# Kernel optimization log

Measured on AMD Instinct MI355X. Metric: run time of the kernel, lower is better.

## Reference

```python
import jax, jax.numpy as jnp
import numpy as np

V = 20000
E = 40000
NODE_IN = 74
EDGE_IN = 12
D = 64            # node_out_feats
EH = 128          # edge_hidden_feats
STEPS = 6         # num_step_message_passing


def setup_inputs() -> dict:
    key = jax.random.key(0)
    ks = jax.random.split(key, 16)
    s = lambda k, shape, scale=0.05: jax.random.normal(k, shape, dtype=jnp.float32) * scale
    return {
        "node_feats": jax.random.normal(ks[0], (V, NODE_IN), dtype=jnp.float32),
        "edge_feats": jax.random.normal(ks[1], (E, EDGE_IN), dtype=jnp.float32),
        "src": jax.random.randint(ks[2], (E,), 0, V),
        "dst": jax.random.randint(ks[3], (E,), 0, V),
        # project_node_feats: Linear(NODE_IN, D) + ReLU
        "proj_W": s(ks[4], (D, NODE_IN)),
        "proj_b": jnp.zeros((D,), jnp.float32),
        # NNConv edge network: Linear(EDGE_IN, EH) -> ReLU -> Linear(EH, D*D)
        "en_W1": s(ks[5], (EH, EDGE_IN)),
        "en_b1": jnp.zeros((EH,), jnp.float32),
        "en_W2": s(ks[6], (D * D, EH)),
        "en_b2": jnp.zeros((D * D,), jnp.float32),
        # NNConv output bias
        "conv_b": jnp.zeros((D,), jnp.float32),
        # single-layer GRU (PyTorch gate order r, z, n)
        "gru_Wih": s(ks[7], (3 * D, D)),
        "gru_Whh": s(ks[8], (3 * D, D)),
        "gru_bih": jnp.zeros((3 * D,), jnp.float32),
        "gru_bhh": jnp.zeros((3 * D,), jnp.float32),
        # MLPPredictor: Linear(2*D, 1)
        "pred_W": s(ks[9], (1, 2 * D)),
        "pred_b": jnp.zeros((1,), jnp.float32),
    }


def reference(node_feats, edge_feats, src, dst, proj_W, proj_b,
              en_W1, en_b1, en_W2, en_b2, conv_b,
              gru_Wih, gru_Whh, gru_bih, gru_bhh, pred_W, pred_b):
    nV = node_feats.shape[0]
    # project node features
    h = jax.nn.relu(node_feats @ proj_W.T + proj_b)  # (V, D)
    # per-edge weight matrices from the edge network (constant across steps)
    ew = jax.nn.relu(edge_feats @ en_W1.T + en_b1) @ en_W2.T + en_b2  # (E, D*D)
    ew = ew.reshape(-1, D, D)  # (E, D, D)

    def step(h, _):
        # NNConv (aggregator='sum'): m_e = h[src_e] @ W_e, sum at dst, + bias
        m = jnp.einsum('ei,eio->eo', h[src], ew)               # (E, D)
        neigh = jax.ops.segment_sum(m, dst, num_segments=nV)   # (V, D)
        x = jax.nn.relu(neigh + conv_b)
        # GRU update; hidden == h (they coincide in the original loop)
        gi = x @ gru_Wih.T + gru_bih
        gh = h @ gru_Whh.T + gru_bhh
        i_r, i_z, i_n = jnp.split(gi, 3, axis=-1)
        h_r, h_z, h_n = jnp.split(gh, 3, axis=-1)
        r = jax.nn.sigmoid(i_r + h_r)
        z = jax.nn.sigmoid(i_z + h_z)
        n = jnp.tanh(i_n + r * h_n)
        h_new = (1.0 - z) * n + z * h
        return h_new, None

    h, _ = jax.lax.scan(step, h, None, length=STEPS)
    # MLPPredictor: per-edge gather-concat-linear
    score = jnp.concatenate([h[src], h[dst]], axis=1) @ pred_W.T + pred_b  # (E, 1)
    return score
```

## Files before the change

### kernel.cpp

```cpp
#include <hip/hip_runtime.h>
#include <hip/hip_bf16.h>
#include <cstdint>

#define NV 20000
#define NE 40000
#define NODE_IN 74
#define EDGE_IN 12
#define D 64
#define EHID 128
#define NSTEPS 6

typedef __bf16 bf16x8 __attribute__((ext_vector_type(8)));
typedef float f32x4 __attribute__((ext_vector_type(4)));

__global__ __launch_bounds__(256) void k_prep(
    const float* __restrict__ nf, const float* __restrict__ pjW, const float* __restrict__ pjb,
    float* __restrict__ h, float* __restrict__ neigh,
    const float* __restrict__ ef, const float* __restrict__ W1, const float* __restrict__ b1,
    __hip_bfloat16* __restrict__ t_bf,
    const float* __restrict__ W2, __hip_bfloat16* __restrict__ w2b,
    const float* __restrict__ b2, __hip_bfloat16* __restrict__ b2t,
    const float* __restrict__ Wih, const float* __restrict__ Whh,
    __hip_bfloat16* __restrict__ Bhi, __hip_bfloat16* __restrict__ Blo) {
  __shared__ float smem[4 * NODE_IN];
  int tid = threadIdx.x;
  int bx = blockIdx.x;
  if (bx < 5000) {
    int nb = bx * 4;
    for (int idx = tid; idx < 4 * NODE_IN; idx += 256)
      smem[idx] = nf[(size_t)nb * NODE_IN + idx];
    __syncthreads();
    int nl = tid >> 6, o = tid & 63;
    float acc = pjb[o];
#pragma unroll
    for (int i = 0; i < NODE_IN; ++i) acc = fmaf(smem[nl * NODE_IN + i], pjW[o * NODE_IN + i], acc);
    h[(size_t)(nb + nl) * D + o] = fmaxf(acc, 0.f);
    neigh[(size_t)(nb + nl) * D + o] = 0.f;
  } else if (bx < 25000) {
    int eb = (bx - 5000) * 2;
    if (tid < 2 * EDGE_IN)
      smem[tid] = ef[(size_t)eb * EDGE_IN + tid];
    __syncthreads();
    int el = tid >> 7, k = tid & 127;
    float acc = b1[k];
#pragma unroll
    for (int j = 0; j < EDGE_IN; ++j) acc = fmaf(smem[el * EDGE_IN + j], W1[k * EDGE_IN + j], acc);
    t_bf[(size_t)(eb + el) * EHID + k] = __float2bfloat16(fmaxf(acc, 0.f));
  } else if (bx < 27048) {
    int idx = (bx - 25000) * 256 + tid;
    w2b[idx] = __float2bfloat16(W2[idx]);
  } else if (bx < 27064) {
    int idx = (bx - 27048) * 256 + tid;
    int o = idx >> 6, i = idx & 63;
    b2t[o * 64 + i] = __float2bfloat16(b2[i * 64 + o]);
  } else {
    int idx = (bx - 27064) * 256 + tid;
    int n = idx >> 7, k = idx & 127;
    int o = n & 63, cls = n >> 6;
    float v;
    if (cls == 0)      v = (k < 64) ? Wih[o * 64 + k]         : Whh[o * 64 + (k - 64)];
    else if (cls == 1) v = (k < 64) ? Wih[(64 + o) * 64 + k]  : Whh[(64 + o) * 64 + (k - 64)];
    else if (cls == 2) v = (k < 64) ? Wih[(128 + o) * 64 + k] : 0.f;
    else               v = (k < 64) ? 0.f                     : Whh[(128 + o) * 64 + (k - 64)];
    __hip_bfloat16 hi = __float2bfloat16(v);
    Bhi[idx] = hi;
    Blo[idx] = __float2bfloat16(v - __bfloat162float(hi));
  }
}

__global__ __launch_bounds__(768, 3) void k_msg(const float* __restrict__ h,
                                                const __hip_bfloat16* __restrict__ t_bf,
                                                const __hip_bfloat16* __restrict__ w2,
                                                const __hip_bfloat16* __restrict__ b2t,
                                                const int* __restrict__ src,
                                                const int* __restrict__ dst,
                                                float* __restrict__ neigh) {
  __shared__ __hip_bfloat16 W2s[512 * 128];
  __shared__ __hip_bfloat16 Hs[12][16 * 64];
  int tid = threadIdx.x;
  int bx = blockIdx.x;
  int cg = bx >> 6, ih = (bx >> 5) & 1, s = bx & 31;
  int lane = tid & 63, lr = lane & 15, lq = lane >> 4;
  int wave = tid >> 6;
  const int ocol = cg * 16 + lr;

  for (int chunk = tid; chunk < 8192; chunk += 768) {
    int row = chunk >> 4, c = chunk & 15;
    int ig = row >> 4, ol = row & 15;
    const __hip_bfloat16* gp =
        w2 + ((size_t)((ih * 32 + ig) * 64 + cg * 16 + ol)) * EHID + c * 8;
    *(bf16x8*)(W2s + row * 128 + ((c ^ ol) * 8)) = *(const bf16x8*)gp;
  }
  bf16x8 b2f0, b2f1;
#pragma unroll
  for (int j = 0; j < 8; ++j) {
    int k = lq * 8 + j;
    __bf16 v = *(const __bf16*)(b2t + (size_t)ocol * 64 + ih * 32 + k);
    __bf16 z = (__bf16)0.0f;
    b2f0[j] = (k < 16) ? v : z;
    b2f1[j] = (k >= 16) ? v : z;
  }
  __syncthreads();

  __hip_bfloat16* Hsw = &Hs[wave][0];
  int e0s = s * 1280;
  int nt = (s < 31) ? 20 : 5;

  int sw0 = (((0 * 4 + lq) ^ lr) * 8);
  int sw1 = (((1 * 4 + lq) ^ lr) * 8);
  int sw2 = (((2 * 4 + lq) ^ lr) * 8);
  int sw3 = (((3 * 4 + lq) ^ lr) * 8);

  int se0 = (wave < nt) ? src[e0s + wave * 64 + lane] : 0;
  int se1 = (wave + 12 < nt) ? src[e0s + (wave + 12) * 64 + lane] : 0;

#pragma unroll 1
  for (int r2 = 0; r2 < 2; ++r2) {
    int t = r2 * 12 + wave;
    if (t >= nt) break;
    int e0t = e0s + t * 64;
    int s_e = r2 ? se1 : se0;

    bf16x8 tf[4][4];
#pragma unroll
    for (int mt = 0; mt < 4; ++mt)
#pragma unroll
      for (int ks = 0; ks < 4; ++ks)
        tf[mt][ks] = *(const bf16x8*)(t_bf + (size_t)(e0t + mt * 16 + lr) * EHID +
                                      ks * 32 + lq * 8);

    int4 dv[4];
#pragma unroll
    for (int mt = 0; mt < 4; ++mt)
      dv[mt] = *(const int4*)(dst + e0t + mt * 16 + lq * 4);

    const float* hrow = h + (size_t)s_e * D + ih * 32;
    f32x4 C[4];
#pragma unroll
    for (int mt = 0; mt < 4; ++mt) C[mt] = f32x4{0.f, 0.f, 0.f, 0.f};

#pragma unroll
    for (int ph = 0; ph < 2; ++ph) {
#pragma unroll
      for (int q = 0; q < 4; ++q) {
        float4 hv = *(const float4*)(hrow + ph * 16 + q * 4);
        Hsw[(q * 4 + 0) * 64 + lane] = __float2bfloat16(hv.x);
        Hsw[(q * 4 + 1) * 64 + lane] = __float2bfloat16(hv.y);
        Hsw[(q * 4 + 2) * 64 + lane] = __float2bfloat16(hv.z);
        Hsw[(q * 4 + 3) * 64 + lane] = __float2bfloat16(hv.w);
      }
#pragma unroll
      for (int mt = 0; mt < 4; ++mt) {
        bf16x8 af;
#pragma unroll
        for (int j = 0; j < 8; ++j)
          af[j] = *(const __bf16*)(Hsw + ((lq * 8 + j) & 15) * 64 + mt * 16 + lr);
        C[mt] = __builtin_amdgcn_mfma_f32_16x16x32_bf16(af, ph ? b2f1 : b2f0, C[mt], 0, 0, 0);
      }
      __builtin_amdgcn_s_setprio(1);
#pragma unroll 2
      for (int igl = 0; igl < 16; ++igl) {
        int ig = ph * 16 + igl;
        const __hip_bfloat16* Wr = W2s + (ig * 16 + lr) * 128;
        bf16x8 f0 = *(const bf16x8*)(Wr + sw0);
        bf16x8 f1 = *(const bf16x8*)(Wr + sw1);
        bf16x8 f2 = *(const bf16x8*)(Wr + sw2);
        bf16x8 f3 = *(const bf16x8*)(Wr + sw3);
#pragma unroll
        for (int mt = 0; mt < 4; ++mt) {
          f32x4 P = {0.f, 0.f, 0.f, 0.f};
          P = __builtin_amdgcn_mfma_f32_16x16x32_bf16(tf[mt][0], f0, P, 0, 0, 0);
          P = __builtin_amdgcn_mfma_f32_16x16x32_bf16(tf[mt][1], f1, P, 0, 0, 0);
          P = __builtin_amdgcn_mfma_f32_16x16x32_bf16(tf[mt][2], f2, P, 0, 0, 0);
          P = __builtin_amdgcn_mfma_f32_16x16x32_bf16(tf[mt][3], f3, P, 0, 0, 0);
          uint2 hA = *(const uint2*)(Hsw + igl * 64 + mt * 16 + lq * 4);
          C[mt][0] = fmaf(__uint_as_float(hA.x << 16), P[0], C[mt][0]);
          C[mt][1] = fmaf(__uint_as_float(hA.x & 0xffff0000u), P[1], C[mt][1]);
          C[mt][2] = fmaf(__uint_as_float(hA.y << 16), P[2], C[mt][2]);
          C[mt][3] = fmaf(__uint_as_float(hA.y & 0xffff0000u), P[3], C[mt][3]);
        }
      }
      __builtin_amdgcn_s_setprio(0);
    }
#pragma unroll
    for (int mt = 0; mt < 4; ++mt) {
      atomicAdd(neigh + (size_t)dv[mt].x * D + ocol, C[mt][0]);
      atomicAdd(neigh + (size_t)dv[mt].y * D + ocol, C[mt][1]);
      atomicAdd(neigh + (size_t)dv[mt].z * D + ocol, C[mt][2]);
      atomicAdd(neigh + (size_t)dv[mt].w * D + ocol, C[mt][3]);
    }
  }
}

__global__ __launch_bounds__(256) void k_gru(float* __restrict__ neigh,
                                             float* __restrict__ h,
                                             const __hip_bfloat16* __restrict__ Bhi,
                                             const __hip_bfloat16* __restrict__ Blo,
                                             const float* __restrict__ cb,
                                             const float* __restrict__ bih,
                                             const float* __restrict__ bhh) {
  __shared__ __hip_bfloat16 Ahi[32 * 128];
  __shared__ __hip_bfloat16 Alo[32 * 128];
  int tid = threadIdx.x;
  int n0 = blockIdx.x * 32;
  for (int idx = tid; idx < 32 * 64; idx += 256) {
    int node = idx >> 6, f = idx & 63;
    int gn = n0 + node;
    float xv = fmaxf(neigh[(size_t)gn * D + f] + cb[f], 0.f);
    neigh[(size_t)gn * D + f] = 0.f;
    float hv = h[(size_t)gn * D + f];
    __hip_bfloat16 xh = __float2bfloat16(xv);
    __hip_bfloat16 hh = __float2bfloat16(hv);
    Ahi[node * 128 + f] = xh;
    Ahi[node * 128 + 64 + f] = hh;
    Alo[node * 128 + f] = __float2bfloat16(xv - __bfloat162float(xh));
    Alo[node * 128 + 64 + f] = __float2bfloat16(hv - __bfloat162float(hh));
  }
  __syncthreads();
  int wave = tid >> 6, lane = tid & 63;
  int lr = lane & 15, lq = lane >> 4;
  f32x4 acc[2][4] = {};
#pragma unroll
  for (int ks = 0; ks < 4; ++ks) {
    int koff = ks * 32 + lq * 8;
    bf16x8 ah[2], al[2], bh[4], bl[4];
#pragma unroll
    for (int mt = 0; mt < 2; ++mt) {
      ah[mt] = *(const bf16x8*)(Ahi + (mt * 16 + lr) * 128 + koff);
      al[mt] = *(const bf16x8*)(Alo + (mt * 16 + lr) * 128 + koff);
    }
#pragma unroll
    for (int cls = 0; cls < 4; ++cls) {
      int n = cls * 64 + wave * 16 + lr;
      bh[cls] = *(const bf16x8*)(Bhi + (size_t)n * 128 + koff);
      bl[cls] = *(const bf16x8*)(Blo + (size_t)n * 128 + koff);
    }
#pragma unroll
    for (int mt = 0; mt < 2; ++mt)
#pragma unroll
      for (int cls = 0; cls < 4; ++cls) {
        acc[mt][cls] = __builtin_amdgcn_mfma_f32_16x16x32_bf16(ah[mt], bh[cls], acc[mt][cls], 0, 0, 0);
        acc[mt][cls] = __builtin_amdgcn_mfma_f32_16x16x32_bf16(al[mt], bh[cls], acc[mt][cls], 0, 0, 0);
        acc[mt][cls] = __builtin_amdgcn_mfma_f32_16x16x32_bf16(ah[mt], bl[cls], acc[mt][cls], 0, 0, 0);
      }
  }
  int o = wave * 16 + lr;
  float b_r = bih[o] + bhh[o];
  float b_z = bih[64 + o] + bhh[64 + o];
  float b_in = bih[128 + o];
  float b_hn = bhh[128 + o];
#pragma unroll
  for (int mt = 0; mt < 2; ++mt) {
#pragma unroll
    for (int r = 0; r < 4; ++r) {
      int gn = n0 + mt * 16 + lq * 4 + r;
      float rs = acc[mt][0][r] + b_r;
      float zs = acc[mt][1][r] + b_z;
      float inn = acc[mt][2][r] + b_in;
      float hnn = acc[mt][3][r] + b_hn;
      float rg = 1.f / (1.f + __expf(-rs));
      float zg = 1.f / (1.f + __expf(-zs));
      float a = inn + rg * hnn;
      a = fminf(fmaxf(a, -15.f), 15.f);
      float e2 = __expf(2.f * a);
      float nn = (e2 - 1.f) / (e2 + 1.f);
      float hold = h[(size_t)gn * D + o];
      h[(size_t)gn * D + o] = (1.f - zg) * nn + zg * hold;
    }
  }
}

__global__ __launch_bounds__(256) void k_pred(const float* __restrict__ h,
                                              const int* __restrict__ src,
                                              const int* __restrict__ dst,
                                              const float* __restrict__ pW,
                                              const float* __restrict__ pb,
                                              float* __restrict__ out) {
  int wave = threadIdx.x >> 6, lane = threadIdx.x & 63;
  int e = blockIdx.x * 4 + wave;
  int s = src[e], d2 = dst[e];
  float v = h[(size_t)s * D + lane] * pW[lane] + h[(size_t)d2 * D + lane] * pW[64 + lane];
#pragma unroll
  for (int off = 32; off >= 1; off >>= 1) v += __shfl_xor(v, off, 64);
  if (lane == 0) out[e] = v + pb[0];
}

extern "C" void kernel_launch(void* const* d_in, const int* in_sizes, int n_in,
                              void* d_out, int out_size, void* d_ws, size_t ws_size,
                              hipStream_t stream) {
  const float* node_feats = (const float*)d_in[0];
  const float* edge_feats = (const float*)d_in[1];
  const int* src = (const int*)d_in[2];
  const int* dst = (const int*)d_in[3];
  const float* proj_W = (const float*)d_in[4];
  const float* proj_b = (const float*)d_in[5];
  const float* en_W1 = (const float*)d_in[6];
  const float* en_b1 = (const float*)d_in[7];
  const float* en_W2 = (const float*)d_in[8];
  const float* en_b2 = (const float*)d_in[9];
  const float* conv_b = (const float*)d_in[10];
  const float* gru_Wih = (const float*)d_in[11];
  const float* gru_Whh = (const float*)d_in[12];
  const float* gru_bih = (const float*)d_in[13];
  const float* gru_bhh = (const float*)d_in[14];
  const float* pred_W = (const float*)d_in[15];
  const float* pred_b = (const float*)d_in[16];

  char* ws = (char*)d_ws;
  size_t off = 0;
  auto walloc = [&](size_t bytes) -> void* {
    void* p = ws + off;
    off = (off + bytes + 255) & ~(size_t)255;
    return p;
  };
  float* h = (float*)walloc((size_t)NV * D * 4);
  float* neigh = (float*)walloc((size_t)NV * D * 4);
  __hip_bfloat16* t_bf = (__hip_bfloat16*)walloc((size_t)NE * EHID * 2);
  __hip_bfloat16* w2_bf = (__hip_bfloat16*)walloc((size_t)D * D * EHID * 2);
  __hip_bfloat16* b2t = (__hip_bfloat16*)walloc((size_t)D * D * 2);
  __hip_bfloat16* Bhi = (__hip_bfloat16*)walloc((size_t)256 * 128 * 2);
  __hip_bfloat16* Blo = (__hip_bfloat16*)walloc((size_t)256 * 128 * 2);

  k_prep<<<27192, 256, 0, stream>>>(node_feats, proj_W, proj_b, h, neigh,
                                    edge_feats, en_W1, en_b1, t_bf,
                                    en_W2, w2_bf, en_b2, b2t,
                                    gru_Wih, gru_Whh, Bhi, Blo);
  for (int s = 0; s < NSTEPS; ++s) {
    k_msg<<<256, 768, 0, stream>>>(h, t_bf, w2_bf, b2t, src, dst, neigh);
    k_gru<<<NV / 32, 256, 0, stream>>>(neigh, h, Bhi, Blo, conv_b, gru_bih, gru_bhh);
  }
  k_pred<<<NE / 4, 256, 0, stream>>>(h, src, dst, pred_W, pred_b, (float*)d_out);
}
```

Measured before the change: 519.3 us.

## Fuse message, GRU and predictor steps into one cooperative persistent kernel

Replaces the per-step k_msg/k_gru launches and the final k_pred with a single cooperative kernel that uses grid.sync between message aggregation and the GRU update. The goal is to remove 13 kernel launch boundaries and their drain/fill gaps. The block shape drops from 768 to 512 threads, so each block runs fewer waves and iterates three edge tiles per wave. The W2 tile in LDS is reloaded each step because the GRU phase reuses that shared memory. Grid-wide syncs cost something, and with 256 blocks the GRU work is spread over only two passes.

```diff
diff --git a/kernel.cpp b/kernel.cpp
--- a/kernel.cpp
+++ b/kernel.cpp
@@ -1,6 +1,9 @@
 #include <hip/hip_runtime.h>
+#include <hip/hip_cooperative_groups.h>
 #include <hip/hip_bf16.h>
 #include <cstdint>
+
+namespace coop = cooperative_groups;
 
 #define NV 20000
 #define NE 40000
@@ -68,29 +71,24 @@
   }
 }
 
-__global__ __launch_bounds__(768, 3) void k_msg(const float* __restrict__ h,
-                                                const __hip_bfloat16* __restrict__ t_bf,
-                                                const __hip_bfloat16* __restrict__ w2,
-                                                const __hip_bfloat16* __restrict__ b2t,
-                                                const int* __restrict__ src,
-                                                const int* __restrict__ dst,
-                                                float* __restrict__ neigh) {
+__global__ __launch_bounds__(512, 2) void k_steps(
+    float* __restrict__ h, const __hip_bfloat16* __restrict__ t_bf,
+    const __hip_bfloat16* __restrict__ w2, const __hip_bfloat16* __restrict__ b2t,
+    const int* __restrict__ src, const int* __restrict__ dst,
+    float* __restrict__ neigh,
+    const __hip_bfloat16* __restrict__ Bhi, const __hip_bfloat16* __restrict__ Blo,
+    const float* __restrict__ cb, const float* __restrict__ bih, const float* __restrict__ bhh,
+    const float* __restrict__ pW, const float* __restrict__ pb, float* __restrict__ out) {
+  coop::grid_group grid = coop::this_grid();
   __shared__ __hip_bfloat16 W2s[512 * 128];
-  __shared__ __hip_bfloat16 Hs[12][16 * 64];
+  __shared__ __hip_bfloat16 Hs[8][16 * 64];
   int tid = threadIdx.x;
   int bx = blockIdx.x;
-  int cg = bx >> 6, ih = (bx >> 5) & 1, s = bx & 31;
+  int og = bx >> 6, ih = (bx >> 5) & 1, s = bx & 31;
   int lane = tid & 63, lr = lane & 15, lq = lane >> 4;
   int wave = tid >> 6;
-  const int ocol = cg * 16 + lr;
-
-  for (int chunk = tid; chunk < 8192; chunk += 768) {
-    int row = chunk >> 4, c = chunk & 15;
-    int ig = row >> 4, ol = row & 15;
-    const __hip_bfloat16* gp =
-        w2 + ((size_t)((ih * 32 + ig) * 64 + cg * 16 + ol)) * EHID + c * 8;
-    *(bf16x8*)(W2s + row * 128 + ((c ^ ol) * 8)) = *(const bf16x8*)gp;
-  }
+  const int ocol = og * 16 + lr;
+
   bf16x8 b2f0, b2f1;
 #pragma unroll
   for (int j = 0; j < 8; ++j) {
@@ -100,189 +98,196 @@
     b2f0[j] = (k < 16) ? v : z;
     b2f1[j] = (k >= 16) ? v : z;
   }
-  __syncthreads();
-
-  __hip_bfloat16* Hsw = &Hs[wave][0];
   int e0s = s * 1280;
   int nt = (s < 31) ? 20 : 5;
-
   int sw0 = (((0 * 4 + lq) ^ lr) * 8);
   int sw1 = (((1 * 4 + lq) ^ lr) * 8);
   int sw2 = (((2 * 4 + lq) ^ lr) * 8);
   int sw3 = (((3 * 4 + lq) ^ lr) * 8);
-
-  int se0 = (wave < nt) ? src[e0s + wave * 64 + lane] : 0;
-  int se1 = (wave + 12 < nt) ? src[e0s + (wave + 12) * 64 + lane] : 0;
+  int se0 = src[e0s + wave * 64 + lane];
+  int se1 = (wave + 8 < nt) ? src[e0s + (wave + 8) * 64 + lane] : 0;
+  int se2 = (wave + 16 < nt) ? src[e0s + (wave + 16) * 64 + lane] : 0;
+  __hip_bfloat16* Hsw = &Hs[wave][0];
+
+  for (int step = 0; step < NSTEPS; ++step) {
+    int nit = step ? 4 : 16;
+    for (int it = 0; it < nit; ++it) {
+      int chunk = it * 512 + tid;
+      int row = chunk >> 4, c = chunk & 15;
+      int ig = row >> 4, ol = row & 15;
+      const __hip_bfloat16* gp =
+          w2 + ((size_t)((ih * 32 + ig) * 64 + og * 16 + ol)) * EHID + c * 8;
+      *(bf16x8*)(W2s + row * 128 + ((c ^ ol) * 8)) = *(const bf16x8*)gp;
+    }
+    __syncthreads();
 
 #pragma unroll 1
-  for (int r2 = 0; r2 < 2; ++r2) {
-    int t = r2 * 12 + wave;
-    if (t >= nt) break;
-    int e0t = e0s + t * 64;
-    int s_e = r2 ? se1 : se0;
-
-    bf16x8 tf[4][4];
-#pragma unroll
-    for (int mt = 0; mt < 4; ++mt)
-#pragma unroll
-      for (int ks = 0; ks < 4; ++ks)
-        tf[mt][ks] = *(const bf16x8*)(t_bf + (size_t)(e0t + mt * 16 + lr) * EHID +
-                                      ks * 32 + lq * 8);
-
-    int4 dv[4];
-#pragma unroll
-    for (int mt = 0; mt < 4; ++mt)
-      dv[mt] = *(const int4*)(dst + e0t + mt * 16 + lq * 4);
-
-    const float* hrow = h + (size_t)s_e * D + ih * 32;
-    f32x4 C[4];
-#pragma unroll
-    for (int mt = 0; mt < 4; ++mt) C[mt] = f32x4{0.f, 0.f, 0.f, 0.f};
-
-#pragma unroll
-    for (int ph = 0; ph < 2; ++ph) {
-#pragma unroll
-      for (int q = 0; q < 4; ++q) {
-        float4 hv = *(const float4*)(hrow + ph * 16 + q * 4);
-        Hsw[(q * 4 + 0) * 64 + lane] = __float2bfloat16(hv.x);
-        Hsw[(q * 4 + 1) * 64 + lane] = __float2bfloat16(hv.y);
-        Hsw[(q * 4 + 2) * 64 + lane] = __float2bfloat16(hv.z);
-        Hsw[(q * 4 + 3) * 64 + lane] = __float2bfloat16(hv.w);
+    for (int r3 = 0; r3 < 3; ++r3) {
+      int t = r3 * 8 + wave;
+      if (t >= nt) break;
+      int e0t = e0s + t * 64;
+      int s_e = (r3 == 0) ? se0 : (r3 == 1) ? se1 : se2;
+
+      bf16x8 tf[4][4];
+#pragma unroll
+      for (int mt = 0; mt < 4; ++mt)
+#pragma unroll
+        for (int ks = 0; ks < 4; ++ks)
+          tf[mt][ks] = *(const bf16x8*)(t_bf + (size_t)(e0t + mt * 16 + lr) * EHID +
+                                        ks * 32 + lq * 8);
+      int4 dv[4];
+#pragma unroll
+      for (int mt = 0; mt < 4; ++mt)
+        dv[mt] = *(const int4*)(dst + e0t + mt * 16 + lq * 4);
+
+      const float* hrow = h + (size_t)s_e * D + ih * 32;
+      f32x4 C[4];
+#pragma unroll
+      for (int mt = 0; mt < 4; ++mt) C[mt] = f32x4{0.f, 0.f, 0.f, 0.f};
+
+#pragma unroll
+      for (int ph = 0; ph < 2; ++ph) {
+#pragma unroll
+        for (int q = 0; q < 4; ++q) {
+          float4 hv = *(const float4*)(hrow + ph * 16 + q * 4);
+          Hsw[(q * 4 + 0) * 64 + lane] = __float2bfloat16(hv.x);
+          Hsw[(q * 4 + 1) * 64 + lane] = __float2bfloat16(hv.y);
+          Hsw[(q * 4 + 2) * 64 + lane] = __float2bfloat16(hv.z);
+          Hsw[(q * 4 + 3) * 64 + lane] = __float2bfloat16(hv.w);
+        }
+#pragma unroll
+        for (int mt = 0; mt < 4; ++mt) {
+          bf16x8 af;
+#pragma unroll
+          for (int j = 0; j < 8; ++j)
+            af[j] = *(const __bf16*)(Hsw + ((lq * 8 + j) & 15) * 64 + mt * 16 + lr);
+          C[mt] = __builtin_amdgcn_mfma_f32_16x16x32_bf16(af, ph ? b2f1 : b2f0, C[mt], 0, 0, 0);
+        }
+        __builtin_amdgcn_s_setprio(1);
+#pragma unroll 2
+        for (int igl = 0; igl < 16; ++igl) {
+          int ig = ph * 16 + igl;
+          const __hip_bfloat16* Wr = W2s + (ig * 16 + lr) * 128;
+          bf16x8 f0 = *(const bf16x8*)(Wr + sw0);
+          bf16x8 f1 = *(const bf16x8*)(Wr + sw1);
+          bf16x8 f2 = *(const bf16x8*)(Wr + sw2);
+          bf16x8 f3 = *(const bf16x8*)(Wr + sw3);
+#pragma unroll
+          for (int mt = 0; mt < 4; ++mt) {
+            f32x4 P = {0.f, 0.f, 0.f, 0.f};
+            P = __builtin_amdgcn_mfma_f32_16x16x32_bf16(tf[mt][0], f0, P, 0, 0, 0);
+            P = __builtin_amdgcn_mfma_f32_16x16x32_bf16(tf[mt][1], f1, P, 0, 0, 0);
+            P = __builtin_amdgcn_mfma_f32_16x16x32_bf16(tf[mt][2], f2, P, 0, 0, 0);
+            P = __builtin_amdgcn_mfma_f32_16x16x32_bf16(tf[mt][3], f3, P, 0, 0, 0);
+            uint2 hA = *(const uint2*)(Hsw + igl * 64 + mt * 16 + lq * 4);
+            C[mt][0] = fmaf(__uint_as_float(hA.x << 16), P[0], C[mt][0]);
+            C[mt][1] = fmaf(__uint_as_float(hA.x & 0xffff0000u), P[1], C[mt][1]);
+            C[mt][2] = fmaf(__uint_as_float(hA.y << 16), P[2], C[mt][2]);
+            C[mt][3] = fmaf(__uint_as_float(hA.y & 0xffff0000u), P[3], C[mt][3]);
+          }
+        }
+        __builtin_amdgcn_s_setprio(0);
       }
 #pragma unroll
       for (int mt = 0; mt < 4; ++mt) {
-        bf16x8 af;
-#pragma unroll
-        for (int j = 0; j < 8; ++j)
-          af[j] = *(const __bf16*)(Hsw + ((lq * 8 + j) & 15) * 64 + mt * 16 + lr);
-        C[mt] = __builtin_amdgcn_mfma_f32_16x16x32_bf16(af, ph ? b2f1 : b2f0, C[mt], 0, 0, 0);
+        atomicAdd(neigh + (size_t)dv[mt].x * D + ocol, C[mt][0]);
+        atomicAdd(neigh + (size_t)dv[mt].y * D + ocol, C[mt][1]);
+        atomicAdd(neigh + (size_t)dv[mt].z * D + ocol, C[mt][2]);
+        atomicAdd(neigh + (size_t)dv[mt].w * D + ocol, C[mt][3]);
       }
-      __builtin_amdgcn_s_setprio(1);
-#pragma unroll 2
-      for (int igl = 0; igl < 16; ++igl) {
-        int ig = ph * 16 + igl;
-        const __hip_bfloat16* Wr = W2s + (ig * 16 + lr) * 128;
-        bf16x8 f0 = *(const bf16x8*)(Wr + sw0);
-        bf16x8 f1 = *(const bf16x8*)(Wr + sw1);
-        bf16x8 f2 = *(const bf16x8*)(Wr + sw2);
-        bf16x8 f3 = *(const bf16x8*)(Wr + sw3);
-#pragma unroll
-        for (int mt = 0; mt < 4; ++mt) {
-          f32x4 P = {0.f, 0.f, 0.f, 0.f};
-          P = __builtin_amdgcn_mfma_f32_16x16x32_bf16(tf[mt][0], f0, P, 0, 0, 0);
-          P = __builtin_amdgcn_mfma_f32_16x16x32_bf16(tf[mt][1], f1, P, 0, 0, 0);
-          P = __builtin_amdgcn_mfma_f32_16x16x32_bf16(tf[mt][2], f2, P, 0, 0, 0);
-          P = __builtin_amdgcn_mfma_f32_16x16x32_bf16(tf[mt][3], f3, P, 0, 0, 0);
-          uint2 hA = *(const uint2*)(Hsw + igl * 64 + mt * 16 + lq * 4);
-          C[mt][0] = fmaf(__uint_as_float(hA.x << 16), P[0], C[mt][0]);
-          C[mt][1] = fmaf(__uint_as_float(hA.x & 0xffff0000u), P[1], C[mt][1]);
-          C[mt][2] = fmaf(__uint_as_float(hA.y << 16), P[2], C[mt][2]);
-          C[mt][3] = fmaf(__uint_as_float(hA.y & 0xffff0000u), P[3], C[mt][3]);
+    }
+    grid.sync();
+
+    int g = tid >> 8;
+    int lt = tid & 255;
+    int wave4 = (tid >> 6) & 3;
+    __hip_bfloat16* Ahi = W2s + g * 8192;
+    __hip_bfloat16* Alo = Ahi + 4096;
+#pragma unroll 1
+    for (int rep = 0; rep < 2; ++rep) {
+      int gg = rep * 512 + bx * 2 + g;
+      if (rep) __syncthreads();
+      if (gg < 625) {
+        int n0 = gg * 32;
+        for (int idx = lt; idx < 32 * 64; idx += 256) {
+          int node = idx >> 6, f = idx & 63;
+          int gn = n0 + node;
+          float xv = fmaxf(neigh[(size_t)gn * D + f] + cb[f], 0.f);
+          neigh[(size_t)gn * D + f] = 0.f;
+          float hv = h[(size_t)gn * D + f];
+          __hip_bfloat16 xh = __float2bfloat16(xv);
+          __hip_bfloat16 hh = __float2bfloat16(hv);
+          Ahi[node * 128 + f] = xh;
+          Ahi[node * 128 + 64 + f] = hh;
+          Alo[node * 128 + f] = __float2bfloat16(xv - __bfloat162float(xh));
+          Alo[node * 128 + 64 + f] = __float2bfloat16(hv - __bfloat162float(hh));
         }
       }
-      __builtin_amdgcn_s_setprio(0);
+      __syncthreads();
+      if (gg < 625) {
+        int n0 = gg * 32;
+        f32x4 acc[2][4] = {};
+#pragma unroll
+        for (int ks = 0; ks < 4; ++ks) {
+          int koff = ks * 32 + lq * 8;
+          bf16x8 ah[2], al[2], bh[4], bl[4];
+#pragma unroll
+          for (int mt = 0; mt < 2; ++mt) {
+            ah[mt] = *(const bf16x8*)(Ahi + (mt * 16 + lr) * 128 + koff);
+            al[mt] = *(const bf16x8*)(Alo + (mt * 16 + lr) * 128 + koff);
+          }
+#pragma unroll
+          for (int cls = 0; cls < 4; ++cls) {
+            int n = cls * 64 + wave4 * 16 + lr;
+            bh[cls] = *(const bf16x8*)(Bhi + (size_t)n * 128 + koff);
+            bl[cls] = *(const bf16x8*)(Blo + (size_t)n * 128 + koff);
+          }
+#pragma unroll
+          for (int mt = 0; mt < 2; ++mt)
+#pragma unroll
+            for (int cls = 0; cls < 4; ++cls) {
+              acc[mt][cls] = __builtin_amdgcn_mfma_f32_16x16x32_bf16(ah[mt], bh[cls], acc[mt][cls], 0, 0, 0);
+              acc[mt][cls] = __builtin_amdgcn_mfma_f32_16x16x32_bf16(al[mt], bh[cls], acc[mt][cls], 0, 0, 0);
+              acc[mt][cls] = __builtin_amdgcn_mfma_f32_16x16x32_bf16(ah[mt], bl[cls], acc[mt][cls], 0, 0, 0);
+            }
+        }
+        int o = wave4 * 16 + lr;
+        float b_r = bih[o] + bhh[o];
+        float b_z = bih[64 + o] + bhh[64 + o];
+        float b_in = bih[128 + o];
+        float b_hn = bhh[128 + o];
+#pragma unroll
+        for (int mt = 0; mt < 2; ++mt) {
+#pragma unroll
+          for (int r = 0; r < 4; ++r) {
+            int gn = n0 + mt * 16 + lq * 4 + r;
+            float rs = acc[mt][0][r] + b_r;
+            float zs = acc[mt][1][r] + b_z;
+            float inn = acc[mt][2][r] + b_in;
+            float hnn = acc[mt][3][r] + b_hn;
+            float rg = 1.f / (1.f + __expf(-rs));
+            float zg = 1.f / (1.f + __expf(-zs));
+            float a = inn + rg * hnn;
+            a = fminf(fmaxf(a, -15.f), 15.f);
+            float e2 = __expf(2.f * a);
+            float nn = (e2 - 1.f) / (e2 + 1.f);
+            float hold = h[(size_t)gn * D + o];
+            h[(size_t)gn * D + o] = (1.f - zg) * nn + zg * hold;
+          }
+        }
+      }
     }
-#pragma unroll
-    for (int mt = 0; mt < 4; ++mt) {
-      atomicAdd(neigh + (size_t)dv[mt].x * D + ocol, C[mt][0]);
-      atomicAdd(neigh + (size_t)dv[mt].y * D + ocol, C[mt][1]);
-      atomicAdd(neigh + (size_t)dv[mt].z * D + ocol, C[mt][2]);
-      atomicAdd(neigh + (size_t)dv[mt].w * D + ocol, C[mt][3]);
-    }
+    grid.sync();
   }
-}
-
-__global__ __launch_bounds__(256) void k_gru(float* __restrict__ neigh,
-                                             float* __restrict__ h,
-                                             const __hip_bfloat16* __restrict__ Bhi,
-                                             const __hip_bfloat16* __restrict__ Blo,
-                                             const float* __restrict__ cb,
-                                             const float* __restrict__ bih,
-                                             const float* __restrict__ bhh) {
-  __shared__ __hip_bfloat16 Ahi[32 * 128];
-  __shared__ __hip_bfloat16 Alo[32 * 128];
-  int tid = threadIdx.x;
-  int n0 = blockIdx.x * 32;
-  for (int idx = tid; idx < 32 * 64; idx += 256) {
-    int node = idx >> 6, f = idx & 63;
-    int gn = n0 + node;
-    float xv = fmaxf(neigh[(size_t)gn * D + f] + cb[f], 0.f);
-    neigh[(size_t)gn * D + f] = 0.f;
-    float hv = h[(size_t)gn * D + f];
-    __hip_bfloat16 xh = __float2bfloat16(xv);
-    __hip_bfloat16 hh = __float2bfloat16(hv);
-    Ahi[node * 128 + f] = xh;
-    Ahi[node * 128 + 64 + f] = hh;
-    Alo[node * 128 + f] = __float2bfloat16(xv - __bfloat162float(xh));
-    Alo[node * 128 + 64 + f] = __float2bfloat16(hv - __bfloat162float(hh));
+
+  int gw = bx * 8 + wave;
+  for (int e = gw; e < NE; e += 2048) {
+    int sE = src[e], dE = dst[e];
+    float v = h[(size_t)sE * D + lane] * pW[lane] + h[(size_t)dE * D + lane] * pW[64 + lane];
+#pragma unroll
+    for (int off = 32; off >= 1; off >>= 1) v += __shfl_xor(v, off, 64);
+    if (lane == 0) out[e] = v + pb[0];
   }
-  __syncthreads();
-  int wave = tid >> 6, lane = tid & 63;
-  int lr = lane & 15, lq = lane >> 4;
-  f32x4 acc[2][4] = {};
-#pragma unroll
-  for (int ks = 0; ks < 4; ++ks) {
-    int koff = ks * 32 + lq * 8;
-    bf16x8 ah[2], al[2], bh[4], bl[4];
-#pragma unroll
-    for (int mt = 0; mt < 2; ++mt) {
-      ah[mt] = *(const bf16x8*)(Ahi + (mt * 16 + lr) * 128 + koff);
-      al[mt] = *(const bf16x8*)(Alo + (mt * 16 + lr) * 128 + koff);
-    }
-#pragma unroll
-    for (int cls = 0; cls < 4; ++cls) {
-      int n = cls * 64 + wave * 16 + lr;
-      bh[cls] = *(const bf16x8*)(Bhi + (size_t)n * 128 + koff);
-      bl[cls] = *(const bf16x8*)(Blo + (size_t)n * 128 + koff);
-    }
-#pragma unroll
-    for (int mt = 0; mt < 2; ++mt)
-#pragma unroll
-      for (int cls = 0; cls < 4; ++cls) {
-        acc[mt][cls] = __builtin_amdgcn_mfma_f32_16x16x32_bf16(ah[mt], bh[cls], acc[mt][cls], 0, 0, 0);
-        acc[mt][cls] = __builtin_amdgcn_mfma_f32_16x16x32_bf16(al[mt], bh[cls], acc[mt][cls], 0, 0, 0);
-        acc[mt][cls] = __builtin_amdgcn_mfma_f32_16x16x32_bf16(ah[mt], bl[cls], acc[mt][cls], 0, 0, 0);
-      }
-  }
-  int o = wave * 16 + lr;
-  float b_r = bih[o] + bhh[o];
-  float b_z = bih[64 + o] + bhh[64 + o];
-  float b_in = bih[128 + o];
-  float b_hn = bhh[128 + o];
-#pragma unroll
-  for (int mt = 0; mt < 2; ++mt) {
-#pragma unroll
-    for (int r = 0; r < 4; ++r) {
-      int gn = n0 + mt * 16 + lq * 4 + r;
-      float rs = acc[mt][0][r] + b_r;
-      float zs = acc[mt][1][r] + b_z;
-      float inn = acc[mt][2][r] + b_in;
-      float hnn = acc[mt][3][r] + b_hn;
-      float rg = 1.f / (1.f + __expf(-rs));
-      float zg = 1.f / (1.f + __expf(-zs));
-      float a = inn + rg * hnn;
-      a = fminf(fmaxf(a, -15.f), 15.f);
-      float e2 = __expf(2.f * a);
-      float nn = (e2 - 1.f) / (e2 + 1.f);
-      float hold = h[(size_t)gn * D + o];
-      h[(size_t)gn * D + o] = (1.f - zg) * nn + zg * hold;
-    }
-  }
-}
-
-__global__ __launch_bounds__(256) void k_pred(const float* __restrict__ h,
-                                              const int* __restrict__ src,
-                                              const int* __restrict__ dst,
-                                              const float* __restrict__ pW,
-                                              const float* __restrict__ pb,
-                                              float* __restrict__ out) {
-  int wave = threadIdx.x >> 6, lane = threadIdx.x & 63;
-  int e = blockIdx.x * 4 + wave;
-  int s = src[e], d2 = dst[e];
-  float v = h[(size_t)s * D + lane] * pW[lane] + h[(size_t)d2 * D + lane] * pW[64 + lane];
-#pragma unroll
-  for (int off = 32; off >= 1; off >>= 1) v += __shfl_xor(v, off, 64);
-  if (lane == 0) out[e] = v + pb[0];
 }
 
 extern "C" void kernel_launch(void* const* d_in, const int* in_sizes, int n_in,
@@ -320,14 +325,16 @@
   __hip_bfloat16* b2t = (__hip_bfloat16*)walloc((size_t)D * D * 2);
   __hip_bfloat16* Bhi = (__hip_bfloat16*)walloc((size_t)256 * 128 * 2);
   __hip_bfloat16* Blo = (__hip_bfloat16*)walloc((size_t)256 * 128 * 2);
+  float* outp = (float*)d_out;
 
   k_prep<<<27192, 256, 0, stream>>>(node_feats, proj_W, proj_b, h, neigh,
                                     edge_feats, en_W1, en_b1, t_bf,
                                     en_W2, w2_bf, en_b2, b2t,
                                     gru_Wih, gru_Whh, Bhi, Blo);
-  for (int s = 0; s < NSTEPS; ++s) {
-    k_msg<<<256, 768, 0, stream>>>(h, t_bf, w2_bf, b2t, src, dst, neigh);
-    k_gru<<<NV / 32, 256, 0, stream>>>(neigh, h, Bhi, Blo, conv_b, gru_bih, gru_bhh);
-  }
-  k_pred<<<NE / 4, 256, 0, stream>>>(h, src, dst, pred_W, pred_b, (float*)d_out);
+  void* args[] = {(void*)&h, (void*)&t_bf, (void*)&w2_bf, (void*)&b2t,
+                  (void*)&src, (void*)&dst, (void*)&neigh,
+                  (void*)&Bhi, (void*)&Blo, (void*)&conv_b,
+                  (void*)&gru_bih, (void*)&gru_bhh,
+                  (void*)&pred_W, (void*)&pred_b, (void*)&outp};
+  hipLaunchCooperativeKernel((void*)k_steps, dim3(256), dim3(512), args, 0, stream);
 }
```

New measurement: 932.1 us. 79.5% more time.
